# Kernel tuning notes

Hardware: AMD Instinct MI355X
Metric: run time of the kernel (lower is better)

The kernel has to match this reference:

```python
import jax, jax.numpy as jnp
import numpy as np

WS = 8          # window size (8x8)
HEADS = 8
DIM_HEAD = 28
SCALE = DIM_HEAD ** -0.5


def _window_partition(t, ws=WS):
    # [b, H, W, c] -> [b, n_windows, ws*ws, c]
    b, H, W, c = t.shape
    t = t.reshape(b, H // ws, ws, W // ws, ws, c)
    t = t.transpose(0, 1, 3, 2, 4, 5)
    return t.reshape(b, (H // ws) * (W // ws), ws * ws, c)


def _window_reverse(t, H, W, ws=WS):
    # [b, n_windows, ws*ws, c] -> [b, H, W, c]
    b = t.shape[0]
    c = t.shape[-1]
    t = t.reshape(b, H // ws, W // ws, ws, ws, c)
    t = t.transpose(0, 1, 3, 2, 4, 5)
    return t.reshape(b, H, W, c)


def _heads_split(t, nh):
    # [b, n, mm, (nh*d)] -> [b, n, nh, mm, d]
    b, n, mm, cd = t.shape
    return t.reshape(b, n, mm, nh, cd // nh).transpose(0, 1, 3, 2, 4)


def setup_inputs() -> dict:
    key = jax.random.key(0)
    ks = jax.random.split(key, 6)
    b, H, W, c = 128, 32, 32, 224
    inner = DIM_HEAD * HEADS  # 224
    return {
        "x": jax.random.normal(ks[0], (b, H, W, c), jnp.float32),
        "Wq": jax.random.normal(ks[1], (c, inner), jnp.float32) * (c ** -0.5),
        "Wkv": jax.random.normal(ks[2], (c, 2 * inner), jnp.float32) * (c ** -0.5),
        "Wout": jax.random.normal(ks[3], (inner, c), jnp.float32) * (inner ** -0.5),
        "bout": jnp.zeros((c,), jnp.float32),
        "pos_emb1": jax.random.normal(ks[4], (1, 1, HEADS // 2, WS * WS, WS * WS), jnp.float32),
        "pos_emb2": jax.random.normal(ks[5], (1, 1, HEADS // 2, 16, 16), jnp.float32),
    }


def reference(x, Wq, Wkv, Wout, bout, pos_emb1, pos_emb2):
    b, H, W, c = x.shape
    nh = HEADS // 2  # heads per branch

    q = x @ Wq                       # [b,H,W,224]
    kv = x @ Wkv
    k, v = jnp.split(kv, 2, axis=-1)

    half = c // 2
    q1, q2 = q[..., :half], q[..., half:]
    k1, k2 = k[..., :half], k[..., half:]
    v1, v2 = v[..., :half], v[..., half:]

    # ----- local branch: attention within each 8x8 window -----
    q1 = _heads_split(_window_partition(q1), nh) * SCALE  # [b,n,nh,64,d]
    k1 = _heads_split(_window_partition(k1), nh)
    v1 = _heads_split(_window_partition(v1), nh)
    sim1 = jnp.einsum('bnhid,bnhjd->bnhij', q1, k1) + pos_emb1
    attn1 = jax.nn.softmax(sim1, axis=-1)
    out1 = jnp.einsum('bnhij,bnhjd->bnhid', attn1, v1)    # [b,n,nh,64,d]
    bN = out1.shape[1]
    out1 = out1.transpose(0, 1, 3, 2, 4).reshape(b, bN, WS * WS, half)

    # ----- global branch: attention across windows (same in-window position) -----
    def part_global(t):
        t = _window_partition(t)                 # [b,n,mm,half]
        t = t.transpose(0, 2, 1, 3)              # [b,mm,n,half]
        return _heads_split(t, nh)               # [b,mm,nh,n,d]
    q2 = part_global(q2) * SCALE
    k2 = part_global(k2)
    v2 = part_global(v2)
    sim2 = jnp.einsum('bnhid,bnhjd->bnhij', q2, k2) + pos_emb2
    attn2 = jax.nn.softmax(sim2, axis=-1)
    out2 = jnp.einsum('bnhij,bnhjd->bnhid', attn2, v2)    # [b,mm,nh,n,d]
    out2 = out2.transpose(0, 1, 3, 2, 4).reshape(b, WS * WS, bN, half)
    out2 = out2.transpose(0, 2, 1, 3)                     # [b,n,mm,half]

    out = jnp.concatenate([out1, out2], axis=-1)          # [b,n,mm,c]
    out = out @ Wout + bout
    return _window_reverse(out, H, W)
```

## Files before the change

### kernel.cpp

```cpp
#include <hip/hip_runtime.h>
#include <stdint.h>

typedef short s8v __attribute__((ext_vector_type(8)));
typedef float f4v __attribute__((ext_vector_type(4)));
typedef unsigned short u16;

#define MFMA16(a, b, c) __builtin_amdgcn_mfma_f32_16x16x32_bf16(a, b, c, 0, 0, 0)
#define SCALE 0.1889822365046136f

__device__ __forceinline__ u16 f2bf(float f) {
  union { float f; uint32_t u; } v;
  v.f = f;
  uint32_t u = v.u;
  u += 0x7fffu + ((u >> 16) & 1u);
  return (u16)(u >> 16);
}

__device__ __forceinline__ void gld_lds16(const void* g, void* l) {
  __builtin_amdgcn_global_load_lds(
      (const __attribute__((address_space(1))) void*)g,
      (__attribute__((address_space(3))) void*)l, 16, 0, 0);
}

__global__ void prep_kernel(const float4* __restrict__ x4,
                            const float* __restrict__ Wq,
                            const float* __restrict__ Wkv,
                            const float* __restrict__ Wout,
                            u16* __restrict__ xb,
                            u16* __restrict__ wqkvt,
                            u16* __restrict__ woutt) {
  const int gsz = gridDim.x * blockDim.x;
  const int gt = blockIdx.x * blockDim.x + threadIdx.x;
  for (int i = gt; i < 7340032; i += gsz) {
    float4 v = x4[i];
    ushort4 o;
    o.x = f2bf(v.x); o.y = f2bf(v.y); o.z = f2bf(v.z); o.w = f2bf(v.w);
    ((ushort4*)xb)[i] = o;
  }
  for (int i = gt; i < 768 * 224; i += gsz) {
    const int n = i / 224, k = i - n * 224;
    float v = 0.f;
    if (n < 224) v = Wq[k * 224 + n];
    else if (n < 672) v = Wkv[k * 448 + (n - 224)];
    wqkvt[i] = f2bf(v);
  }
  for (int i = gt; i < 256 * 224; i += gsz) {
    const int n = i / 224, k = i - n * 224;
    const float v = (n < 224) ? Wout[k * 224 + n] : 0.f;
    woutt[i] = f2bf(v);
  }
}

template <int OUT_F32, int NTILES>
__global__ __launch_bounds__(256) void gemm_an(const u16* __restrict__ A,
                                               const u16* __restrict__ Bt,
                                               void* __restrict__ Cp,
                                               const float* __restrict__ bias,
                                               int Nvalid, int ldc) {
  extern __shared__ u16 smem[];
  u16* As  = smem;
  u16* Bs0 = smem + 28672;
  u16* Bs1 = smem + 32768;
  const int tid = threadIdx.x;
  const int wave = tid >> 6, lane = tid & 63;
  const int c16 = lane & 15, g = lane >> 4;
  const int m0 = blockIdx.x * 128;
  const int wm = wave & 1, wn = wave >> 1;

  const int fbw = wave * 1024 + lane * 16;
  for (int rnd = 0; rnd < 14; ++rnd) {
    const int fb = rnd * 4096 + fbw;
    const int row = fb / 448;
    const int off = fb - row * 448;
    gld_lds16(A + (size_t)(m0 + row) * 224 + (off >> 1),
              (char*)As + rnd * 4096 + wave * 1024);
  }

  const int brow0 = fbw >> 6, bcol0 = (fbw & 63) >> 1;

#define STAGE_B(ntile, ktile, bufp)                                            \
  do {                                                                         \
    char* bb = (char*)((bufp) ? Bs1 : Bs0) + wave * 1024;                      \
    const u16* src =                                                           \
        Bt + (size_t)((ntile) * 128 + brow0) * 224 + (ktile) * 32 + bcol0;     \
    gld_lds16(src, bb);                                                        \
    gld_lds16(src + (size_t)64 * 224, bb + 4096);                              \
  } while (0)

  STAGE_B(0, 0, 0);
  if (NTILES * 7 > 1) STAGE_B(0, 1, 1);
  __syncthreads();

  for (int nt = 0; nt < NTILES; ++nt) {
    f4v acc[4][4] = {};
    for (int kt = 0; kt < 7; ++kt) {
      const int t = nt * 7 + kt;
      const u16* Bs = (t & 1) ? Bs1 : Bs0;
      s8v af[4], bf[4];
      for (int tt = 0; tt < 4; ++tt)
        af[tt] = *(const s8v*)&As[(wm * 64 + tt * 16 + c16) * 224 + kt * 32 + g * 8];
      for (int tt = 0; tt < 4; ++tt)
        bf[tt] = *(const s8v*)&Bs[(wn * 64 + tt * 16 + c16) * 32 + g * 8];
      for (int i = 0; i < 4; ++i)
        for (int j = 0; j < 4; ++j)
          acc[i][j] = MFMA16(af[i], bf[j], acc[i][j]);
      __syncthreads();
      const int ns = t + 2;
      if (ns < NTILES * 7) {
        const int nnt = ns / 7;
        STAGE_B(nnt, ns - nnt * 7, t & 1);
      }
    }
    const int n0 = nt * 128;
    for (int i = 0; i < 4; ++i) {
      const int rowb = m0 + wm * 64 + i * 16 + g * 4;
      for (int j = 0; j < 4; ++j) {
        const int col = n0 + wn * 64 + j * 16 + c16;
        if (col < Nvalid) {
          if (OUT_F32) {
            const float bz = bias[col];
            for (int r = 0; r < 4; ++r)
              ((float*)Cp)[(size_t)(rowb + r) * ldc + col] = acc[i][j][r] + bz;
          } else {
            for (int r = 0; r < 4; ++r)
              ((u16*)Cp)[(size_t)(rowb + r) * ldc + col] = f2bf(acc[i][j][r]);
          }
        }
      }
    }
  }
#undef STAGE_B
}

__global__ __launch_bounds__(256) void attn_local(const u16* __restrict__ qkv,
                                                  const float* __restrict__ pos1,
                                                  u16* __restrict__ attn) {
  extern __shared__ u16 sm[];
  u16* qs = sm;
  u16* ks = sm + 8192;
  u16* vt = sm + 18432;
  u16* pm = sm;
  const int blk = blockIdx.x;
  const int b = blk >> 4, win = blk & 15;
  const int wy = win >> 2, wx = win & 3;
  const int tid = threadIdx.x;
  const int base_s = (b * 32 + wy * 8) * 32 + wx * 8;
  for (int idx = tid; idx < 3584; idx += 256) {
    const int mtx = idx / 1792;
    int rem = idx - mtx * 1792;
    const int h = rem / 448; rem -= h * 448;
    const int t = rem / 7;
    const int c4 = rem - t * 7;
    const int s = base_s + (t >> 3) * 32 + (t & 7);
    const ushort4 v = *(const ushort4*)(qkv + (size_t)s * 672 + mtx * 224 + h * 28 + c4 * 4);
    *(ushort4*)((mtx ? ks : qs) + (h * 64 + t) * 32 + c4 * 4) = v;
  }
  for (int idx = tid; idx < 512; idx += 256) {
    const int mtx = idx >> 8;
    const int h = (idx >> 6) & 3, t = idx & 63;
    const ushort4 z = {0, 0, 0, 0};
    *(ushort4*)((mtx ? ks : qs) + (h * 64 + t) * 32 + 28) = z;
  }
  for (int idx = tid; idx < 1792; idx += 256) {
    const int h = idx / 448;
    int rem = idx - h * 448;
    const int t = rem / 7;
    const int c4 = rem - t * 7;
    const int s = base_s + (t >> 3) * 32 + (t & 7);
    const ushort4 v = *(const ushort4*)(qkv + (size_t)s * 672 + 448 + h * 28 + c4 * 4);
    u16* col = vt + (h * 32 + c4 * 4) * 72 + t;
    col[0] = v.x; col[72] = v.y; col[144] = v.z; col[216] = v.w;
  }
  __syncthreads();
  const int h = tid >> 6, lane = tid & 63;
  const int c16 = lane & 15, g = lane >> 4;
  s8v af[4], bf[4];
  for (int t = 0; t < 4; ++t) af[t] = *(const s8v*)&qs[(h * 64 + t * 16 + c16) * 32 + g * 8];
  for (int t = 0; t < 4; ++t) bf[t] = *(const s8v*)&ks[(h * 64 + t * 16 + c16) * 32 + g * 8];
  const f4v fz = {0.f, 0.f, 0.f, 0.f};
  f4v sc[4][4];
  for (int i = 0; i < 4; ++i)
    for (int j = 0; j < 4; ++j)
      sc[i][j] = MFMA16(af[i], bf[j], fz);
  float lrow[4][4];
  const float* ph = pos1 + h * 4096;
  for (int i = 0; i < 4; ++i) {
    for (int r = 0; r < 4; ++r) {
      const int irow = i * 16 + g * 4 + r;
      float mx = -1e30f;
      for (int j = 0; j < 4; ++j) {
        const float v = sc[i][j][r] * SCALE + ph[irow * 64 + j * 16 + c16];
        sc[i][j][r] = v;
        mx = fmaxf(mx, v);
      }
      for (int d = 1; d < 16; d <<= 1) mx = fmaxf(mx, __shfl_xor(mx, d, 64));
      float sum = 0.f;
      for (int j = 0; j < 4; ++j) {
        const float e = __expf(sc[i][j][r] - mx);
        sc[i][j][r] = e;
        sum += e;
      }
      for (int d = 1; d < 16; d <<= 1) sum += __shfl_xor(sum, d, 64);
      lrow[i][r] = sum;
    }
  }
  __syncthreads();
  for (int i = 0; i < 4; ++i)
    for (int r = 0; r < 4; ++r) {
      const int irow = i * 16 + g * 4 + r;
      for (int j = 0; j < 4; ++j)
        pm[(h * 64 + irow) * 72 + j * 16 + c16] = f2bf(sc[i][j][r]);
    }
  f4v o[4][2] = {};
  for (int kk = 0; kk < 2; ++kk) {
    s8v ap[4], bv[2];
    for (int t = 0; t < 4; ++t)
      ap[t] = *(const s8v*)&pm[(h * 64 + t * 16 + c16) * 72 + kk * 32 + g * 8];
    for (int t = 0; t < 2; ++t)
      bv[t] = *(const s8v*)&vt[(h * 32 + t * 16 + c16) * 72 + kk * 32 + g * 8];
    for (int i = 0; i < 4; ++i)
      for (int j = 0; j < 2; ++j)
        o[i][j] = MFMA16(ap[i], bv[j], o[i][j]);
  }
  for (int i = 0; i < 4; ++i)
    for (int r = 0; r < 4; ++r) {
      const int irow = i * 16 + g * 4 + r;
      const int s = base_s + (irow >> 3) * 32 + (irow & 7);
      const float inv = 1.f / lrow[i][r];
      for (int j = 0; j < 2; ++j) {
        const int d = j * 16 + c16;
        if (d < 28)
          attn[(size_t)s * 224 + h * 28 + d] = f2bf(o[i][j][r] * inv);
      }
    }
}

__global__ __launch_bounds__(256) void attn_global(const u16* __restrict__ qkv,
                                                   const float* __restrict__ pos2,
                                                   u16* __restrict__ attn) {
  extern __shared__ u16 smg[];
  u16* qs = smg;
  u16* ks = smg + 8192;
  u16* vt = smg + 16384;
  u16* p2 = smg + 24576;
  const int blk = blockIdx.x;
  const int b = blk >> 4, ig = blk & 15;
  const int tid = threadIdx.x;
  for (int idx = tid; idx < 5376; idx += 256) {
    const int seg = idx / 1792;
    int rem = idx - seg * 1792;
    const int row = rem / 28;
    const int c4 = rem - row * 28;
    const int w = row >> 4, j = row & 15;
    const int ii = ig * 4 + w;
    const int y = ii >> 3, x = ii & 7;
    const int s = (b * 32 + (j >> 2) * 8 + y) * 32 + (j & 3) * 8 + x;
    const int hq = c4 / 7, d4 = c4 - hq * 7;
    const ushort4 v = *(const ushort4*)(qkv + (size_t)s * 672 + 112 + seg * 224 + c4 * 4);
    if (seg < 2) {
      *(ushort4*)((seg ? ks : qs) + ((w * 4 + hq) * 16 + j) * 32 + d4 * 4) = v;
    } else {
      u16* col = vt + ((w * 4 + hq) * 32 + d4 * 4) * 16 + j;
      col[0] = v.x; col[16] = v.y; col[32] = v.z; col[48] = v.w;
    }
  }
  for (int idx = tid; idx < 512; idx += 256) {
    const ushort4 z = {0, 0, 0, 0};
    *(ushort4*)(((idx & 256) ? ks : qs) + (idx & 255) * 32 + 28) = z;
  }
  {
    const ushort4 z = {0, 0, 0, 0};
    const int w = tid >> 6, hq = (tid >> 4) & 3;
    const int dd = 28 + ((tid >> 2) & 3), j4 = tid & 3;
    *(ushort4*)(vt + ((w * 4 + hq) * 32 + dd) * 16 + j4 * 4) = z;
  }
  __syncthreads();
  const int w = tid >> 6, lane = tid & 63;
  const int c16 = lane & 15, g = lane >> 4;
  const int i = ig * 4 + w;
  const int y = i >> 3, x = i & 7;
  const int w4 = w * 4;
  const f4v fz = {0.f, 0.f, 0.f, 0.f};
  for (int h = 0; h < 4; ++h) {
    const s8v aq = *(const s8v*)&qs[((w4 + h) * 16 + c16) * 32 + g * 8];
    const s8v bk = *(const s8v*)&ks[((w4 + h) * 16 + c16) * 32 + g * 8];
    const f4v s = MFMA16(aq, bk, fz);
    const float* ph = pos2 + h * 256;
    float l[4];
    for (int r = 0; r < 4; ++r) {
      const float v = s[r] * SCALE + ph[(g * 4 + r) * 16 + c16];
      float mx = v;
      for (int d = 1; d < 16; d <<= 1) mx = fmaxf(mx, __shfl_xor(mx, d, 64));
      const float e = __expf(v - mx);
      float sum = e;
      for (int d = 1; d < 16; d <<= 1) sum += __shfl_xor(sum, d, 64);
      l[r] = sum;
      p2[(w * 16 + g * 4 + r) * 32 + c16] = f2bf(e);
      p2[(w * 16 + g * 4 + r) * 32 + c16 + 16] = 0;
    }
    const s8v ap = *(const s8v*)&p2[(w * 16 + c16) * 32 + g * 8];
    f4v o[2];
    for (int nt = 0; nt < 2; ++nt) {
      s8v bv = {0, 0, 0, 0, 0, 0, 0, 0};
      if (g < 2)
        bv = *(const s8v*)&vt[((w4 + h) * 32 + nt * 16 + c16) * 16 + g * 8];
      o[nt] = MFMA16(ap, bv, fz);
    }
    for (int nt = 0; nt < 2; ++nt)
      for (int r = 0; r < 4; ++r) {
        const int d = nt * 16 + c16;
        if (d < 28) {
          const int wi = g * 4 + r;
          const int sw = (b * 32 + (wi >> 2) * 8 + y) * 32 + (wi & 3) * 8 + x;
          attn[(size_t)sw * 224 + 112 + h * 28 + d] = f2bf(o[nt][r] / l[r]);
        }
      }
  }
}

extern "C" void kernel_launch(void* const* d_in, const int* in_sizes, int n_in,
                              void* d_out, int out_size, void* d_ws, size_t ws_size,
                              hipStream_t stream) {
  const float* x    = (const float*)d_in[0];
  const float* Wq   = (const float*)d_in[1];
  const float* Wkv  = (const float*)d_in[2];
  const float* Wout = (const float*)d_in[3];
  const float* bout = (const float*)d_in[4];
  const float* pos1 = (const float*)d_in[5];
  const float* pos2 = (const float*)d_in[6];
  char* ws = (char*)d_ws;
  u16* qkv   = (u16*)ws;
  u16* xb    = (u16*)(ws + 176160768);
  u16* attn  = xb;
  u16* wqkvt = (u16*)(ws + 234881024);
  u16* woutt = (u16*)(ws + 235225088);

  prep_kernel<<<dim3(1024), 256, 0, stream>>>(
      (const float4*)x, Wq, Wkv, Wout, xb, wqkvt, woutt);

  gemm_an<0, 6><<<dim3(1024), 256, 73728, stream>>>(xb, wqkvt, qkv, nullptr, 672, 672);

  attn_local<<<dim3(2048), 256, 55296, stream>>>(qkv, pos1, attn);
  attn_global<<<dim3(2048), 256, 53248, stream>>>(qkv, pos2, attn);

  gemm_an<1, 2><<<dim3(1024), 256, 73728, stream>>>(attn, woutt, d_out, bout, 224, 224);
}
```

Baseline: 425.9 us.

## Fuse x fp32-to-bf16 conversion into QKV GEMM and keep A fragments in registers

The separate pass that converts x to bf16 is removed. The QKV GEMM now loads fp32 x directly and converts each A fragment to bf16 in registers. The A tile is no longer staged in LDS; every wave keeps all seven k-slices of its A fragments resident in VGPRs. This cuts LDS from 72KB to 16KB and sets launch bounds to allow two blocks per CU, removing a full read/write round trip of x through memory. The cost is heavy register pressure from 28 s8v fragments plus 16 accumulators, which risks spills, and uncoalesced-ish direct global reads of A.

```diff
diff --git a/kernel.cpp b/kernel.cpp
--- a/kernel.cpp
+++ b/kernel.cpp
@@ -22,21 +22,13 @@
       (__attribute__((address_space(3))) void*)l, 16, 0, 0);
 }
 
-__global__ void prep_kernel(const float4* __restrict__ x4,
-                            const float* __restrict__ Wq,
+__global__ void prep_kernel(const float* __restrict__ Wq,
                             const float* __restrict__ Wkv,
                             const float* __restrict__ Wout,
-                            u16* __restrict__ xb,
                             u16* __restrict__ wqkvt,
                             u16* __restrict__ woutt) {
   const int gsz = gridDim.x * blockDim.x;
   const int gt = blockIdx.x * blockDim.x + threadIdx.x;
-  for (int i = gt; i < 7340032; i += gsz) {
-    float4 v = x4[i];
-    ushort4 o;
-    o.x = f2bf(v.x); o.y = f2bf(v.y); o.z = f2bf(v.z); o.w = f2bf(v.w);
-    ((ushort4*)xb)[i] = o;
-  }
   for (int i = gt; i < 768 * 224; i += gsz) {
     const int n = i / 224, k = i - n * 224;
     float v = 0.f;
@@ -51,16 +43,15 @@
   }
 }
 
-template <int OUT_F32, int NTILES>
-__global__ __launch_bounds__(256) void gemm_an(const u16* __restrict__ A,
-                                               const u16* __restrict__ Bt,
-                                               void* __restrict__ Cp,
-                                               const float* __restrict__ bias,
-                                               int Nvalid, int ldc) {
+template <int A_F32, int OUT_F32, int NTILES>
+__global__ __launch_bounds__(256, 2) void gemm_ar(const void* __restrict__ Ap,
+                                                  const u16* __restrict__ Bt,
+                                                  void* __restrict__ Cp,
+                                                  const float* __restrict__ bias,
+                                                  int Nvalid, int ldc) {
   extern __shared__ u16 smem[];
-  u16* As  = smem;
-  u16* Bs0 = smem + 28672;
-  u16* Bs1 = smem + 32768;
+  u16* Bs0 = smem;
+  u16* Bs1 = smem + 4096;
   const int tid = threadIdx.x;
   const int wave = tid >> 6, lane = tid & 63;
   const int c16 = lane & 15, g = lane >> 4;
@@ -68,14 +59,6 @@
   const int wm = wave & 1, wn = wave >> 1;
 
   const int fbw = wave * 1024 + lane * 16;
-  for (int rnd = 0; rnd < 14; ++rnd) {
-    const int fb = rnd * 4096 + fbw;
-    const int row = fb / 448;
-    const int off = fb - row * 448;
-    gld_lds16(A + (size_t)(m0 + row) * 224 + (off >> 1),
-              (char*)As + rnd * 4096 + wave * 1024);
-  }
-
   const int brow0 = fbw >> 6, bcol0 = (fbw & 63) >> 1;
 
 #define STAGE_B(ntile, ktile, bufp)                                            \
@@ -89,21 +72,47 @@
 
   STAGE_B(0, 0, 0);
   if (NTILES * 7 > 1) STAGE_B(0, 1, 1);
+
+  s8v af[7][4];
+#pragma unroll
+  for (int kt = 0; kt < 7; ++kt) {
+#pragma unroll
+    for (int t = 0; t < 4; ++t) {
+      const int row = m0 + wm * 64 + t * 16 + c16;
+      if (A_F32) {
+        const float* ap = (const float*)Ap + (size_t)row * 224 + kt * 32 + g * 8;
+        const float4 lo = *(const float4*)ap;
+        const float4 hi = *(const float4*)(ap + 4);
+        s8v v;
+        v[0] = (short)f2bf(lo.x); v[1] = (short)f2bf(lo.y);
+        v[2] = (short)f2bf(lo.z); v[3] = (short)f2bf(lo.w);
+        v[4] = (short)f2bf(hi.x); v[5] = (short)f2bf(hi.y);
+        v[6] = (short)f2bf(hi.z); v[7] = (short)f2bf(hi.w);
+        af[kt][t] = v;
+      } else {
+        af[kt][t] = *(const s8v*)((const u16*)Ap + (size_t)row * 224 + kt * 32 + g * 8);
+      }
+    }
+  }
+
   __syncthreads();
 
+#pragma unroll
   for (int nt = 0; nt < NTILES; ++nt) {
     f4v acc[4][4] = {};
+#pragma unroll
     for (int kt = 0; kt < 7; ++kt) {
       const int t = nt * 7 + kt;
       const u16* Bs = (t & 1) ? Bs1 : Bs0;
-      s8v af[4], bf[4];
-      for (int tt = 0; tt < 4; ++tt)
-        af[tt] = *(const s8v*)&As[(wm * 64 + tt * 16 + c16) * 224 + kt * 32 + g * 8];
+      s8v bf[4];
+#pragma unroll
       for (int tt = 0; tt < 4; ++tt)
         bf[tt] = *(const s8v*)&Bs[(wn * 64 + tt * 16 + c16) * 32 + g * 8];
+#pragma unroll
       for (int i = 0; i < 4; ++i)
+#pragma unroll
         for (int j = 0; j < 4; ++j)
-          acc[i][j] = MFMA16(af[i], bf[j], acc[i][j]);
+          acc[i][j] = MFMA16(af[kt][i], bf[j], acc[i][j]);
       __syncthreads();
       const int ns = t + 2;
       if (ns < NTILES * 7) {
@@ -112,8 +121,10 @@
       }
     }
     const int n0 = nt * 128;
+#pragma unroll
     for (int i = 0; i < 4; ++i) {
       const int rowb = m0 + wm * 64 + i * 16 + g * 4;
+#pragma unroll
       for (int j = 0; j < 4; ++j) {
         const int col = n0 + wn * 64 + j * 16 + c16;
         if (col < Nvalid) {
@@ -330,18 +341,16 @@
   const float* pos2 = (const float*)d_in[6];
   char* ws = (char*)d_ws;
   u16* qkv   = (u16*)ws;
-  u16* xb    = (u16*)(ws + 176160768);
-  u16* attn  = xb;
+  u16* attn  = (u16*)(ws + 176160768);
   u16* wqkvt = (u16*)(ws + 234881024);
   u16* woutt = (u16*)(ws + 235225088);
 
-  prep_kernel<<<dim3(1024), 256, 0, stream>>>(
-      (const float4*)x, Wq, Wkv, Wout, xb, wqkvt, woutt);
-
-  gemm_an<0, 6><<<dim3(1024), 256, 73728, stream>>>(xb, wqkvt, qkv, nullptr, 672, 672);
+  prep_kernel<<<dim3(128), 256, 0, stream>>>(Wq, Wkv, Wout, wqkvt, woutt);
+
+  gemm_ar<1, 0, 6><<<dim3(1024), 256, 16384, stream>>>(x, wqkvt, qkv, nullptr, 672, 672);
 
   attn_local<<<dim3(2048), 256, 55296, stream>>>(qkv, pos1, attn);
   attn_global<<<dim3(2048), 256, 53248, stream>>>(qkv, pos2, attn);
 
-  gemm_an<1, 2><<<dim3(1024), 256, 73728, stream>>>(attn, woutt, d_out, bout, 224, 224);
-}
+  gemm_ar<0, 1, 2><<<dim3(1024), 256, 16384, stream>>>(attn, woutt, d_out, bout, 224, 224);
+}
```

Measured after the change: 513.9 us. +20.7%, slower.

## Fuse x fp32-to-bf16 conversion into QKV GEMM and merge attention kernels

Applied to the files above, without the earlier changes.

The QKV GEMM now loads fp32 x directly, converts it to bf16 in registers and writes the tile into LDS, so the separate prep pass over x and its bf16 intermediate buffer go away. The local and global attention kernels are merged into one launch that picks its branch by block index. This removes a full read and write of x plus one kernel launch. The trade-off is that the A-tile load in the GEMM becomes synchronous register traffic instead of async global-to-LDS copies.

```diff
diff --git a/kernel.cpp b/kernel.cpp
--- a/kernel.cpp
+++ b/kernel.cpp
@@ -22,21 +22,13 @@
       (__attribute__((address_space(3))) void*)l, 16, 0, 0);
 }
 
-__global__ void prep_kernel(const float4* __restrict__ x4,
-                            const float* __restrict__ Wq,
+__global__ void prep_kernel(const float* __restrict__ Wq,
                             const float* __restrict__ Wkv,
                             const float* __restrict__ Wout,
-                            u16* __restrict__ xb,
                             u16* __restrict__ wqkvt,
                             u16* __restrict__ woutt) {
   const int gsz = gridDim.x * blockDim.x;
   const int gt = blockIdx.x * blockDim.x + threadIdx.x;
-  for (int i = gt; i < 7340032; i += gsz) {
-    float4 v = x4[i];
-    ushort4 o;
-    o.x = f2bf(v.x); o.y = f2bf(v.y); o.z = f2bf(v.z); o.w = f2bf(v.w);
-    ((ushort4*)xb)[i] = o;
-  }
   for (int i = gt; i < 768 * 224; i += gsz) {
     const int n = i / 224, k = i - n * 224;
     float v = 0.f;
@@ -51,8 +43,8 @@
   }
 }
 
-template <int OUT_F32, int NTILES>
-__global__ __launch_bounds__(256) void gemm_an(const u16* __restrict__ A,
+template <int A_F32, int OUT_F32, int NTILES>
+__global__ __launch_bounds__(256) void gemm_af(const void* __restrict__ Ap,
                                                const u16* __restrict__ Bt,
                                                void* __restrict__ Cp,
                                                const float* __restrict__ bias,
@@ -68,14 +60,6 @@
   const int wm = wave & 1, wn = wave >> 1;
 
   const int fbw = wave * 1024 + lane * 16;
-  for (int rnd = 0; rnd < 14; ++rnd) {
-    const int fb = rnd * 4096 + fbw;
-    const int row = fb / 448;
-    const int off = fb - row * 448;
-    gld_lds16(A + (size_t)(m0 + row) * 224 + (off >> 1),
-              (char*)As + rnd * 4096 + wave * 1024);
-  }
-
   const int brow0 = fbw >> 6, bcol0 = (fbw & 63) >> 1;
 
 #define STAGE_B(ntile, ktile, bufp)                                            \
@@ -89,6 +73,27 @@
 
   STAGE_B(0, 0, 0);
   if (NTILES * 7 > 1) STAGE_B(0, 1, 1);
+
+  if (A_F32) {
+    const float* Af = (const float*)Ap + (size_t)m0 * 224;
+#pragma unroll
+    for (int rnd = 0; rnd < 28; ++rnd) {
+      const int e0 = rnd * 1024 + tid * 4;
+      const float4 v = *(const float4*)(Af + e0);
+      ushort4 o;
+      o.x = f2bf(v.x); o.y = f2bf(v.y); o.z = f2bf(v.z); o.w = f2bf(v.w);
+      *(ushort4*)(As + e0) = o;
+    }
+  } else {
+    for (int rnd = 0; rnd < 14; ++rnd) {
+      const int fb = rnd * 4096 + fbw;
+      const int row = fb / 448;
+      const int off = fb - row * 448;
+      gld_lds16((const u16*)Ap + (size_t)(m0 + row) * 224 + (off >> 1),
+                (char*)As + rnd * 4096 + wave * 1024);
+    }
+  }
+
   __syncthreads();
 
   for (int nt = 0; nt < NTILES; ++nt) {
@@ -132,18 +137,16 @@
 #undef STAGE_B
 }
 
-__global__ __launch_bounds__(256) void attn_local(const u16* __restrict__ qkv,
-                                                  const float* __restrict__ pos1,
-                                                  u16* __restrict__ attn) {
-  extern __shared__ u16 sm[];
+__device__ __forceinline__ void attn_local_body(u16* sm, int blk, int tid,
+                                                const u16* __restrict__ qkv,
+                                                const float* __restrict__ pos1,
+                                                u16* __restrict__ attn) {
   u16* qs = sm;
   u16* ks = sm + 8192;
   u16* vt = sm + 18432;
   u16* pm = sm;
-  const int blk = blockIdx.x;
   const int b = blk >> 4, win = blk & 15;
   const int wy = win >> 2, wx = win & 3;
-  const int tid = threadIdx.x;
   const int base_s = (b * 32 + wy * 8) * 32 + wx * 8;
   for (int idx = tid; idx < 3584; idx += 256) {
     const int mtx = idx / 1792;
@@ -235,17 +238,15 @@
     }
 }
 
-__global__ __launch_bounds__(256) void attn_global(const u16* __restrict__ qkv,
-                                                   const float* __restrict__ pos2,
-                                                   u16* __restrict__ attn) {
-  extern __shared__ u16 smg[];
+__device__ __forceinline__ void attn_global_body(u16* smg, int blk, int tid,
+                                                 const u16* __restrict__ qkv,
+                                                 const float* __restrict__ pos2,
+                                                 u16* __restrict__ attn) {
   u16* qs = smg;
   u16* ks = smg + 8192;
   u16* vt = smg + 16384;
   u16* p2 = smg + 24576;
-  const int blk = blockIdx.x;
   const int b = blk >> 4, ig = blk & 15;
-  const int tid = threadIdx.x;
   for (int idx = tid; idx < 5376; idx += 256) {
     const int seg = idx / 1792;
     int rem = idx - seg * 1792;
@@ -318,6 +319,19 @@
   }
 }
 
+__global__ __launch_bounds__(256) void attn_fused(const u16* __restrict__ qkv,
+                                                  const float* __restrict__ pos1,
+                                                  const float* __restrict__ pos2,
+                                                  u16* __restrict__ attn) {
+  extern __shared__ u16 sm[];
+  const int blk = blockIdx.x;
+  const int tid = threadIdx.x;
+  if (blk < 2048)
+    attn_local_body(sm, blk, tid, qkv, pos1, attn);
+  else
+    attn_global_body(sm, blk - 2048, tid, qkv, pos2, attn);
+}
+
 extern "C" void kernel_launch(void* const* d_in, const int* in_sizes, int n_in,
                               void* d_out, int out_size, void* d_ws, size_t ws_size,
                               hipStream_t stream) {
@@ -330,18 +344,15 @@
   const float* pos2 = (const float*)d_in[6];
   char* ws = (char*)d_ws;
   u16* qkv   = (u16*)ws;
-  u16* xb    = (u16*)(ws + 176160768);
-  u16* attn  = xb;
+  u16* attn  = (u16*)(ws + 176160768);
   u16* wqkvt = (u16*)(ws + 234881024);
   u16* woutt = (u16*)(ws + 235225088);
 
-  prep_kernel<<<dim3(1024), 256, 0, stream>>>(
-      (const float4*)x, Wq, Wkv, Wout, xb, wqkvt, woutt);
-
-  gemm_an<0, 6><<<dim3(1024), 256, 73728, stream>>>(xb, wqkvt, qkv, nullptr, 672, 672);
-
-  attn_local<<<dim3(2048), 256, 55296, stream>>>(qkv, pos1, attn);
-  attn_global<<<dim3(2048), 256, 53248, stream>>>(qkv, pos2, attn);
-
-  gemm_an<1, 2><<<dim3(1024), 256, 73728, stream>>>(attn, woutt, d_out, bout, 224, 224);
-}
+  prep_kernel<<<dim3(128), 256, 0, stream>>>(Wq, Wkv, Wout, wqkvt, woutt);
+
+  gemm_af<1, 0, 6><<<dim3(1024), 256, 73728, stream>>>(x, wqkvt, qkv, nullptr, 672, 672);
+
+  attn_fused<<<dim3(4096), 256, 55296, stream>>>(qkv, pos1, pos2, attn);
+
+  gemm_af<0, 1, 2><<<dim3(1024), 256, 73728, stream>>>(attn, woutt, d_out, bout, 224, 224);
+}
```

Result: no change. 429.7 us (+0.9%).

## Fuse QKV projection into merged local/global attention kernel

Applied to the files above, without the earlier changes.

Removes the separate QKV GEMM and its bf16 qkv intermediate in global memory. A single launch now handles both local and global attention blocks: each block gathers its 64 rows of x, computes only the 336 Q/K/V columns its branch needs with MFMA, and writes them straight into LDS for the attention step. This drops a large global write and read round trip and two launches. The cost is a GEMM whose tiles are only 64 rows tall, which reuses the weights less, and 2 waves/SIMD launch bounds with about 70KB of LDS that may limit occupancy. The output GEMM also issues its B-tile loads before its A-tile loads.

```diff
diff --git a/kernel.cpp b/kernel.cpp
--- a/kernel.cpp
+++ b/kernel.cpp
@@ -52,7 +52,7 @@
 }
 
 template <int OUT_F32, int NTILES>
-__global__ __launch_bounds__(256) void gemm_an(const u16* __restrict__ A,
+__global__ __launch_bounds__(256) void gemm_af(const u16* __restrict__ Ap,
                                                const u16* __restrict__ Bt,
                                                void* __restrict__ Cp,
                                                const float* __restrict__ bias,
@@ -68,14 +68,6 @@
   const int wm = wave & 1, wn = wave >> 1;
 
   const int fbw = wave * 1024 + lane * 16;
-  for (int rnd = 0; rnd < 14; ++rnd) {
-    const int fb = rnd * 4096 + fbw;
-    const int row = fb / 448;
-    const int off = fb - row * 448;
-    gld_lds16(A + (size_t)(m0 + row) * 224 + (off >> 1),
-              (char*)As + rnd * 4096 + wave * 1024);
-  }
-
   const int brow0 = fbw >> 6, bcol0 = (fbw & 63) >> 1;
 
 #define STAGE_B(ntile, ktile, bufp)                                            \
@@ -89,6 +81,14 @@
 
   STAGE_B(0, 0, 0);
   if (NTILES * 7 > 1) STAGE_B(0, 1, 1);
+
+  for (int rnd = 0; rnd < 14; ++rnd) {
+    const int fb = rnd * 4096 + fbw;
+    const int row = fb / 448;
+    const int off = fb - row * 448;
+    gld_lds16(Ap + (size_t)(m0 + row) * 224 + (off >> 1),
+              (char*)As + rnd * 4096 + wave * 1024);
+  }
   __syncthreads();
 
   for (int nt = 0; nt < NTILES; ++nt) {
@@ -132,190 +132,242 @@
 #undef STAGE_B
 }
 
-__global__ __launch_bounds__(256) void attn_local(const u16* __restrict__ qkv,
-                                                  const float* __restrict__ pos1,
-                                                  u16* __restrict__ attn) {
+__global__ __launch_bounds__(256, 2) void attn_fused(
+    const u16* __restrict__ xb, const u16* __restrict__ Wt,
+    const float* __restrict__ pos1, const float* __restrict__ pos2,
+    u16* __restrict__ attn) {
   extern __shared__ u16 sm[];
-  u16* qs = sm;
-  u16* ks = sm + 8192;
-  u16* vt = sm + 18432;
-  u16* pm = sm;
-  const int blk = blockIdx.x;
-  const int b = blk >> 4, win = blk & 15;
-  const int wy = win >> 2, wx = win & 3;
+  u16* As  = sm;
+  u16* Bs0 = sm + 14336;
+  u16* Bs1 = sm + 25088;
+  const int blk0 = blockIdx.x;
+  const int local = (blk0 < 2048) ? 1 : 0;
+  const int blk = local ? blk0 : blk0 - 2048;
   const int tid = threadIdx.x;
-  const int base_s = (b * 32 + wy * 8) * 32 + wx * 8;
-  for (int idx = tid; idx < 3584; idx += 256) {
-    const int mtx = idx / 1792;
-    int rem = idx - mtx * 1792;
-    const int h = rem / 448; rem -= h * 448;
-    const int t = rem / 7;
-    const int c4 = rem - t * 7;
-    const int s = base_s + (t >> 3) * 32 + (t & 7);
-    const ushort4 v = *(const ushort4*)(qkv + (size_t)s * 672 + mtx * 224 + h * 28 + c4 * 4);
-    *(ushort4*)((mtx ? ks : qs) + (h * 64 + t) * 32 + c4 * 4) = v;
-  }
-  for (int idx = tid; idx < 512; idx += 256) {
-    const int mtx = idx >> 8;
-    const int h = (idx >> 6) & 3, t = idx & 63;
-    const ushort4 z = {0, 0, 0, 0};
-    *(ushort4*)((mtx ? ks : qs) + (h * 64 + t) * 32 + 28) = z;
-  }
-  for (int idx = tid; idx < 1792; idx += 256) {
-    const int h = idx / 448;
-    int rem = idx - h * 448;
-    const int t = rem / 7;
-    const int c4 = rem - t * 7;
-    const int s = base_s + (t >> 3) * 32 + (t & 7);
-    const ushort4 v = *(const ushort4*)(qkv + (size_t)s * 672 + 448 + h * 28 + c4 * 4);
-    u16* col = vt + (h * 32 + c4 * 4) * 72 + t;
-    col[0] = v.x; col[72] = v.y; col[144] = v.z; col[216] = v.w;
-  }
+  const int wave = tid >> 6, lane = tid & 63;
+  const int c16 = lane & 15, g = lane >> 4;
+  const int b = blk >> 4, sub = blk & 15;
+
+  int base_s = 0, ig = 0;
+  if (local) {
+    base_s = (b * 32 + (sub >> 2) * 8) * 32 + (sub & 3) * 8;
+  } else {
+    ig = sub;
+  }
+
+#pragma unroll
+  for (int m = 0; m < 7; ++m) {
+    const int chunk = m * 256 + tid;
+    const int row = chunk / 28;
+    const int c = chunk - row * 28;
+    int s;
+    if (local) {
+      s = base_s + (row >> 3) * 32 + (row & 7);
+    } else {
+      const int w2 = row >> 4, j = row & 15;
+      const int ii = ig * 4 + w2;
+      const int y = ii >> 3, x = ii & 7;
+      s = (b * 32 + (j >> 2) * 8 + y) * 32 + (j & 3) * 8 + x;
+    }
+    gld_lds16(xb + (size_t)s * 224 + c * 8, (char*)As + chunk * 16);
+  }
+
+  const int qoff = local ? 0 : 112;
+#define STAGE_W(ktile, buf)                                                   \
+  do {                                                                        \
+    for (int mm = 0; mm < 6; ++mm) {                                          \
+      const int ch = mm * 256 + tid;                                          \
+      if (ch < 1344) {                                                        \
+        const int brow = ch >> 2, bc = (ch & 3) * 8;                          \
+        const int n = qoff + brow + ((brow >= 112) ? 112 : 0) +               \
+                      ((brow >= 224) ? 112 : 0);                              \
+        gld_lds16(Wt + (size_t)n * 224 + (ktile) * 32 + bc,                   \
+                  (char*)(buf) + ch * 16);                                    \
+      }                                                                       \
+    }                                                                         \
+  } while (0)
+
+  STAGE_W(0, Bs0);
+  STAGE_W(1, Bs1);
   __syncthreads();
-  const int h = tid >> 6, lane = tid & 63;
-  const int c16 = lane & 15, g = lane >> 4;
-  s8v af[4], bf[4];
-  for (int t = 0; t < 4; ++t) af[t] = *(const s8v*)&qs[(h * 64 + t * 16 + c16) * 32 + g * 8];
-  for (int t = 0; t < 4; ++t) bf[t] = *(const s8v*)&ks[(h * 64 + t * 16 + c16) * 32 + g * 8];
-  const f4v fz = {0.f, 0.f, 0.f, 0.f};
-  f4v sc[4][4];
-  for (int i = 0; i < 4; ++i)
-    for (int j = 0; j < 4; ++j)
-      sc[i][j] = MFMA16(af[i], bf[j], fz);
-  float lrow[4][4];
-  const float* ph = pos1 + h * 4096;
-  for (int i = 0; i < 4; ++i) {
-    for (int r = 0; r < 4; ++r) {
-      const int irow = i * 16 + g * 4 + r;
-      float mx = -1e30f;
-      for (int j = 0; j < 4; ++j) {
-        const float v = sc[i][j][r] * SCALE + ph[irow * 64 + j * 16 + c16];
-        sc[i][j][r] = v;
-        mx = fmaxf(mx, v);
-      }
-      for (int d = 1; d < 16; d <<= 1) mx = fmaxf(mx, __shfl_xor(mx, d, 64));
-      float sum = 0.f;
-      for (int j = 0; j < 4; ++j) {
-        const float e = __expf(sc[i][j][r] - mx);
-        sc[i][j][r] = e;
-        sum += e;
-      }
-      for (int d = 1; d < 16; d <<= 1) sum += __shfl_xor(sum, d, 64);
-      lrow[i][r] = sum;
-    }
-  }
-  __syncthreads();
-  for (int i = 0; i < 4; ++i)
-    for (int r = 0; r < 4; ++r) {
-      const int irow = i * 16 + g * 4 + r;
-      for (int j = 0; j < 4; ++j)
-        pm[(h * 64 + irow) * 72 + j * 16 + c16] = f2bf(sc[i][j][r]);
-    }
-  f4v o[4][2] = {};
-  for (int kk = 0; kk < 2; ++kk) {
-    s8v ap[4], bv[2];
-    for (int t = 0; t < 4; ++t)
-      ap[t] = *(const s8v*)&pm[(h * 64 + t * 16 + c16) * 72 + kk * 32 + g * 8];
-    for (int t = 0; t < 2; ++t)
-      bv[t] = *(const s8v*)&vt[(h * 32 + t * 16 + c16) * 72 + kk * 32 + g * 8];
-    for (int i = 0; i < 4; ++i)
-      for (int j = 0; j < 2; ++j)
-        o[i][j] = MFMA16(ap[i], bv[j], o[i][j]);
-  }
-  for (int i = 0; i < 4; ++i)
-    for (int r = 0; r < 4; ++r) {
-      const int irow = i * 16 + g * 4 + r;
-      const int s = base_s + (irow >> 3) * 32 + (irow & 7);
-      const float inv = 1.f / lrow[i][r];
-      for (int j = 0; j < 2; ++j) {
-        const int d = j * 16 + c16;
-        if (d < 28)
-          attn[(size_t)s * 224 + h * 28 + d] = f2bf(o[i][j][r] * inv);
-      }
-    }
-}
-
-__global__ __launch_bounds__(256) void attn_global(const u16* __restrict__ qkv,
-                                                   const float* __restrict__ pos2,
-                                                   u16* __restrict__ attn) {
-  extern __shared__ u16 smg[];
-  u16* qs = smg;
-  u16* ks = smg + 8192;
-  u16* vt = smg + 16384;
-  u16* p2 = smg + 24576;
-  const int blk = blockIdx.x;
-  const int b = blk >> 4, ig = blk & 15;
-  const int tid = threadIdx.x;
-  for (int idx = tid; idx < 5376; idx += 256) {
-    const int seg = idx / 1792;
-    int rem = idx - seg * 1792;
-    const int row = rem / 28;
-    const int c4 = rem - row * 28;
-    const int w = row >> 4, j = row & 15;
-    const int ii = ig * 4 + w;
-    const int y = ii >> 3, x = ii & 7;
-    const int s = (b * 32 + (j >> 2) * 8 + y) * 32 + (j & 3) * 8 + x;
-    const int hq = c4 / 7, d4 = c4 - hq * 7;
-    const ushort4 v = *(const ushort4*)(qkv + (size_t)s * 672 + 112 + seg * 224 + c4 * 4);
-    if (seg < 2) {
-      *(ushort4*)((seg ? ks : qs) + ((w * 4 + hq) * 16 + j) * 32 + d4 * 4) = v;
-    } else {
-      u16* col = vt + ((w * 4 + hq) * 32 + d4 * 4) * 16 + j;
-      col[0] = v.x; col[16] = v.y; col[32] = v.z; col[48] = v.w;
-    }
-  }
-  for (int idx = tid; idx < 512; idx += 256) {
-    const ushort4 z = {0, 0, 0, 0};
-    *(ushort4*)(((idx & 256) ? ks : qs) + (idx & 255) * 32 + 28) = z;
+
+  f4v acc[6][4] = {};
+  for (int kt = 0; kt < 7; ++kt) {
+    const u16* Bs = (kt & 1) ? Bs1 : Bs0;
+    s8v af[4];
+#pragma unroll
+    for (int st = 0; st < 4; ++st)
+      af[st] = *(const s8v*)&As[(st * 16 + c16) * 224 + kt * 32 + g * 8];
+#pragma unroll
+    for (int j = 0; j < 6; ++j) {
+      const int tile = j * 4 + wave;
+      if (tile < 21) {
+        const s8v bf = *(const s8v*)&Bs[(tile * 16 + c16) * 32 + g * 8];
+#pragma unroll
+        for (int st = 0; st < 4; ++st)
+          acc[j][st] = MFMA16(af[st], bf, acc[j][st]);
+      }
+    }
+    __syncthreads();
+    if (kt + 2 < 7) STAGE_W(kt + 2, (kt & 1) ? Bs1 : Bs0);
+  }
+
+  u16* qs  = sm;
+  u16* ks  = sm + 8192;
+  u16* vtL = sm + 18432;
+  u16* vtG = sm + 16384;
+  u16* pm  = sm;
+  u16* p2  = sm + 24608;
+
+#pragma unroll
+  for (int j = 0; j < 6; ++j) {
+    const int tile = j * 4 + wave;
+    if (tile < 21) {
+      const int seg = (tile >= 14) ? 2 : ((tile >= 7) ? 1 : 0);
+      const int nn = tile * 16 + c16 - seg * 112;
+      const int h = ((nn >= 28) ? 1 : 0) + ((nn >= 56) ? 1 : 0) + ((nn >= 84) ? 1 : 0);
+      const int d = nn - h * 28;
+#pragma unroll
+      for (int st = 0; st < 4; ++st) {
+        if (seg == 2) {
+          ushort4 o;
+          o.x = f2bf(acc[j][st][0]); o.y = f2bf(acc[j][st][1]);
+          o.z = f2bf(acc[j][st][2]); o.w = f2bf(acc[j][st][3]);
+          if (local)
+            *(ushort4*)&vtL[(h * 32 + d) * 72 + st * 16 + g * 4] = o;
+          else
+            *(ushort4*)&vtG[st * 2056 + (h * 32 + d) * 16 + g * 4] = o;
+        } else {
+          u16* dst = seg ? ks : qs;
+#pragma unroll
+          for (int r = 0; r < 4; ++r) {
+            const u16 v = f2bf(acc[j][st][r]);
+            if (local)
+              dst[(h * 64 + st * 16 + g * 4 + r) * 32 + d] = v;
+            else
+              dst[((st * 4 + h) * 16 + g * 4 + r) * 32 + d] = v;
+          }
+        }
+      }
+    }
   }
   {
     const ushort4 z = {0, 0, 0, 0};
-    const int w = tid >> 6, hq = (tid >> 4) & 3;
-    const int dd = 28 + ((tid >> 2) & 3), j4 = tid & 3;
-    *(ushort4*)(vt + ((w * 4 + hq) * 32 + dd) * 16 + j4 * 4) = z;
+    *(ushort4*)(qs + tid * 32 + 28) = z;
+    *(ushort4*)(ks + tid * 32 + 28) = z;
+    if (!local) {
+      const int w2 = tid >> 6, hq = (tid >> 4) & 3;
+      const int dd = 28 + ((tid >> 2) & 3), j4 = tid & 3;
+      *(ushort4*)(vtG + w2 * 2056 + (hq * 32 + dd) * 16 + j4 * 4) = z;
+    }
   }
   __syncthreads();
-  const int w = tid >> 6, lane = tid & 63;
-  const int c16 = lane & 15, g = lane >> 4;
-  const int i = ig * 4 + w;
-  const int y = i >> 3, x = i & 7;
-  const int w4 = w * 4;
+
   const f4v fz = {0.f, 0.f, 0.f, 0.f};
-  for (int h = 0; h < 4; ++h) {
-    const s8v aq = *(const s8v*)&qs[((w4 + h) * 16 + c16) * 32 + g * 8];
-    const s8v bk = *(const s8v*)&ks[((w4 + h) * 16 + c16) * 32 + g * 8];
-    const f4v s = MFMA16(aq, bk, fz);
-    const float* ph = pos2 + h * 256;
-    float l[4];
-    for (int r = 0; r < 4; ++r) {
-      const float v = s[r] * SCALE + ph[(g * 4 + r) * 16 + c16];
-      float mx = v;
-      for (int d = 1; d < 16; d <<= 1) mx = fmaxf(mx, __shfl_xor(mx, d, 64));
-      const float e = __expf(v - mx);
-      float sum = e;
-      for (int d = 1; d < 16; d <<= 1) sum += __shfl_xor(sum, d, 64);
-      l[r] = sum;
-      p2[(w * 16 + g * 4 + r) * 32 + c16] = f2bf(e);
-      p2[(w * 16 + g * 4 + r) * 32 + c16 + 16] = 0;
-    }
-    const s8v ap = *(const s8v*)&p2[(w * 16 + c16) * 32 + g * 8];
-    f4v o[2];
-    for (int nt = 0; nt < 2; ++nt) {
-      s8v bv = {0, 0, 0, 0, 0, 0, 0, 0};
-      if (g < 2)
-        bv = *(const s8v*)&vt[((w4 + h) * 32 + nt * 16 + c16) * 16 + g * 8];
-      o[nt] = MFMA16(ap, bv, fz);
-    }
-    for (int nt = 0; nt < 2; ++nt)
+  if (local) {
+    const int h = wave;
+    s8v af2[4], bf2[4];
+    for (int t = 0; t < 4; ++t)
+      af2[t] = *(const s8v*)&qs[(h * 64 + t * 16 + c16) * 32 + g * 8];
+    for (int t = 0; t < 4; ++t)
+      bf2[t] = *(const s8v*)&ks[(h * 64 + t * 16 + c16) * 32 + g * 8];
+    f4v sc[4][4];
+    for (int i = 0; i < 4; ++i)
+      for (int j = 0; j < 4; ++j)
+        sc[i][j] = MFMA16(af2[i], bf2[j], fz);
+    float lrow[4][4];
+    const float* ph = pos1 + h * 4096;
+    for (int i = 0; i < 4; ++i) {
       for (int r = 0; r < 4; ++r) {
-        const int d = nt * 16 + c16;
-        if (d < 28) {
-          const int wi = g * 4 + r;
-          const int sw = (b * 32 + (wi >> 2) * 8 + y) * 32 + (wi & 3) * 8 + x;
-          attn[(size_t)sw * 224 + 112 + h * 28 + d] = f2bf(o[nt][r] / l[r]);
-        }
-      }
-  }
+        const int irow = i * 16 + g * 4 + r;
+        float mx = -1e30f;
+        for (int j = 0; j < 4; ++j) {
+          const float v = sc[i][j][r] * SCALE + ph[irow * 64 + j * 16 + c16];
+          sc[i][j][r] = v;
+          mx = fmaxf(mx, v);
+        }
+        for (int dd = 1; dd < 16; dd <<= 1) mx = fmaxf(mx, __shfl_xor(mx, dd, 64));
+        float sum = 0.f;
+        for (int j = 0; j < 4; ++j) {
+          const float e = __expf(sc[i][j][r] - mx);
+          sc[i][j][r] = e;
+          sum += e;
+        }
+        for (int dd = 1; dd < 16; dd <<= 1) sum += __shfl_xor(sum, dd, 64);
+        lrow[i][r] = sum;
+      }
+    }
+    __syncthreads();
+    for (int i = 0; i < 4; ++i)
+      for (int r = 0; r < 4; ++r) {
+        const int irow = i * 16 + g * 4 + r;
+        for (int j = 0; j < 4; ++j)
+          pm[(h * 64 + irow) * 72 + j * 16 + c16] = f2bf(sc[i][j][r]);
+      }
+    f4v o[4][2] = {};
+    for (int kk = 0; kk < 2; ++kk) {
+      s8v ap[4], bv[2];
+      for (int t = 0; t < 4; ++t)
+        ap[t] = *(const s8v*)&pm[(h * 64 + t * 16 + c16) * 72 + kk * 32 + g * 8];
+      for (int t = 0; t < 2; ++t)
+        bv[t] = *(const s8v*)&vtL[(h * 32 + t * 16 + c16) * 72 + kk * 32 + g * 8];
+      for (int i = 0; i < 4; ++i)
+        for (int j = 0; j < 2; ++j)
+          o[i][j] = MFMA16(ap[i], bv[j], o[i][j]);
+    }
+    for (int i = 0; i < 4; ++i)
+      for (int r = 0; r < 4; ++r) {
+        const int irow = i * 16 + g * 4 + r;
+        const int s = base_s + (irow >> 3) * 32 + (irow & 7);
+        const float inv = 1.f / lrow[i][r];
+        for (int j = 0; j < 2; ++j) {
+          const int d = j * 16 + c16;
+          if (d < 28)
+            attn[(size_t)s * 224 + h * 28 + d] = f2bf(o[i][j][r] * inv);
+        }
+      }
+  } else {
+    const int w = wave;
+    const int i = ig * 4 + w;
+    const int y = i >> 3, x = i & 7;
+    const int w4 = w * 4;
+    for (int h = 0; h < 4; ++h) {
+      const s8v aq = *(const s8v*)&qs[((w4 + h) * 16 + c16) * 32 + g * 8];
+      const s8v bk = *(const s8v*)&ks[((w4 + h) * 16 + c16) * 32 + g * 8];
+      const f4v s = MFMA16(aq, bk, fz);
+      const float* ph = pos2 + h * 256;
+      float l[4];
+      for (int r = 0; r < 4; ++r) {
+        const float v = s[r] * SCALE + ph[(g * 4 + r) * 16 + c16];
+        float mx = v;
+        for (int dd = 1; dd < 16; dd <<= 1) mx = fmaxf(mx, __shfl_xor(mx, dd, 64));
+        const float e = __expf(v - mx);
+        float sum = e;
+        for (int dd = 1; dd < 16; dd <<= 1) sum += __shfl_xor(sum, dd, 64);
+        l[r] = sum;
+        p2[(w * 16 + g * 4 + r) * 32 + c16] = f2bf(e);
+        p2[(w * 16 + g * 4 + r) * 32 + c16 + 16] = 0;
+      }
+      const s8v ap = *(const s8v*)&p2[(w * 16 + c16) * 32 + g * 8];
+      f4v o[2];
+      for (int nt = 0; nt < 2; ++nt) {
+        s8v bv = {0, 0, 0, 0, 0, 0, 0, 0};
+        if (g < 2)
+          bv = *(const s8v*)&vtG[w * 2056 + (h * 32 + nt * 16 + c16) * 16 + g * 8];
+        o[nt] = MFMA16(ap, bv, fz);
+      }
+      for (int nt = 0; nt < 2; ++nt)
+        for (int r = 0; r < 4; ++r) {
+          const int d = nt * 16 + c16;
+          if (d < 28) {
+            const int wi = g * 4 + r;
+            const int sw = (b * 32 + (wi >> 2) * 8 + y) * 32 + (wi & 3) * 8 + x;
+            attn[(size_t)sw * 224 + 112 + h * 28 + d] = f2bf(o[nt][r] / l[r]);
+          }
+        }
+    }
+  }
+#undef STAGE_W
 }
 
 extern "C" void kernel_launch(void* const* d_in, const int* in_sizes, int n_in,
@@ -329,19 +381,15 @@
   const float* pos1 = (const float*)d_in[5];
   const float* pos2 = (const float*)d_in[6];
   char* ws = (char*)d_ws;
-  u16* qkv   = (u16*)ws;
-  u16* xb    = (u16*)(ws + 176160768);
-  u16* attn  = xb;
-  u16* wqkvt = (u16*)(ws + 234881024);
-  u16* woutt = (u16*)(ws + 235225088);
+  u16* xb    = (u16*)ws;
+  u16* attn  = (u16*)(ws + 58720256);
+  u16* wqkvt = (u16*)(ws + 117440512);
+  u16* woutt = (u16*)(ws + 117784576);
 
   prep_kernel<<<dim3(1024), 256, 0, stream>>>(
       (const float4*)x, Wq, Wkv, Wout, xb, wqkvt, woutt);
 
-  gemm_an<0, 6><<<dim3(1024), 256, 73728, stream>>>(xb, wqkvt, qkv, nullptr, 672, 672);
-
-  attn_local<<<dim3(2048), 256, 55296, stream>>>(qkv, pos1, attn);
-  attn_global<<<dim3(2048), 256, 53248, stream>>>(qkv, pos2, attn);
-
-  gemm_an<1, 2><<<dim3(1024), 256, 73728, stream>>>(attn, woutt, d_out, bout, 224, 224);
-}
+  attn_fused<<<dim3(4096), 256, 71680, stream>>>(xb, wqkvt, pos1, pos2, attn);
+
+  gemm_af<1, 2><<<dim3(1024), 256, 73728, stream>>>(attn, woutt, d_out, bout, 224, 224);
+}
```

Result: faster. 368.8 us (-13.4%).
